# Performance work log

Hardware: AMD Instinct MI355X
Metric: run time of the kernel (lower is better)

Reference implementation:

```python
import jax, jax.numpy as jnp
import numpy as np

N_NODES = 50000
N_EDGES = 800000
F_IN = 128
HID = 128
N_GRAPHS = 256


def setup_inputs() -> dict:
    key = jax.random.key(0)
    ks = jax.random.split(key, 12)
    gx = jax.random.normal(ks[0], (N_NODES, F_IN), dtype=jnp.float32)
    edge_index = jax.random.randint(ks[1], (2, N_EDGES), 0, N_NODES, dtype=jnp.int64)
    batch = jnp.sort(jax.random.randint(ks[2], (N_NODES,), 0, N_GRAPHS, dtype=jnp.int64))
    edge_attr = jax.random.uniform(ks[3], (N_EDGES,), dtype=jnp.float32)
    s1 = 1.0 / np.sqrt(F_IN)
    s2 = 1.0 / np.sqrt(HID)
    W1 = jax.random.uniform(ks[4], (F_IN, HID), jnp.float32, -s1, s1)
    b1 = jnp.zeros((HID,), jnp.float32)
    W2 = jax.random.uniform(ks[5], (HID, HID), jnp.float32, -s2, s2)
    b2 = jnp.zeros((HID,), jnp.float32)
    W3 = jax.random.uniform(ks[6], (HID, HID), jnp.float32, -s2, s2)
    b3 = jnp.zeros((HID,), jnp.float32)
    return {"gx": gx, "edge_index": edge_index, "batch": batch, "edge_attr": edge_attr,
            "W1": W1, "b1": b1, "W2": W2, "b2": b2, "W3": W3, "b3": b3}


def _gcn_conv(x, W, b, row, col, edge_weight, n_nodes):
    # PyG GCNConv with add_self_loops=False:
    #   deg[i] = sum of edge_weight over edges with dst == i
    #   norm_e = deg^{-1/2}[row] * w_e * deg^{-1/2}[col]
    #   out[i] = sum_{e: col_e == i} norm_e * (x @ W)[row_e] + b
    deg = jax.ops.segment_sum(edge_weight, col, num_segments=n_nodes)
    dinv = jnp.where(deg > 0, jax.lax.rsqrt(deg), 0.0)
    norm = dinv[row] * edge_weight * dinv[col]  # [E]
    h = x @ W  # [N, H]
    msg = h[row] * norm[:, None]  # [E, H] gather + scale
    out = jax.ops.segment_sum(msg, col, num_segments=n_nodes)  # scatter-add
    return out + b


def reference(gx, edge_index, batch, edge_attr, W1, b1, W2, b2, W3, b3):
    row, col = edge_index[0], edge_index[1]
    n = gx.shape[0]
    # dropout layers are in eval mode (identity) for a deterministic reference
    h = jax.nn.relu(_gcn_conv(gx, W1, b1, row, col, edge_attr, n))
    h = jax.nn.relu(_gcn_conv(h, W2, b2, row, col, edge_attr, n))
    h = _gcn_conv(h, W3, b3, row, col, edge_attr, n)
    readout = jax.ops.segment_sum(h, batch, num_segments=N_GRAPHS)  # global_add_pool
    return h, readout
```

## Files before the change

### kernel.cpp

```cpp
#include <hip/hip_runtime.h>

#define FEAT 128

typedef __attribute__((ext_vector_type(8))) short short8;
typedef __attribute__((ext_vector_type(4))) float f32x4;

__device__ __forceinline__ unsigned int bf16rtn(float f) {
    unsigned int u = __float_as_uint(f);
    return (u + 0x7fffu + ((u >> 16) & 1u)) >> 16;
}
__device__ __forceinline__ float bf16tof(unsigned int h) { return __uint_as_float(h << 16); }
__device__ __forceinline__ float bf16lo(unsigned int v) { return __uint_as_float(v << 16); }
__device__ __forceinline__ float bf16hi(unsigned int v) { return __uint_as_float(v & 0xffff0000u); }

__global__ __launch_bounds__(256) void hist_kernel(const int* __restrict__ col,
                                                   int* __restrict__ ghist,
                                                   const float* __restrict__ W0,
                                                   const float* __restrict__ W1,
                                                   const float* __restrict__ W2,
                                                   unsigned short* __restrict__ Whi,
                                                   unsigned short* __restrict__ Wlo,
                                                   int E, int nblk, int nbuck) {
    __shared__ int h[256];
    const int t = threadIdx.x, b = blockIdx.x;
// ... 76 lines not shown
    if (t < nbuck) {
        int idx = t * nblk + b;
        cur[t] = gsc[idx] + sbs[idx >> 8];
    }
    __syncthreads();
    const int base = b * 4096;
#pragma unroll
    for (int i = 0; i < 16; ++i) {
        int e = base + i * 256 + t;
        if (e < E) {
            int c = col[e];
            int slot = atomicAdd(&cur[c >> 8], 1);
            bedge[slot] = make_uint2(((unsigned)c << 16) | (unsigned)row[e],
                                     __float_as_uint(ew[e]));
        }
    }
}

__global__ __launch_bounds__(256) void bucket_kernel(const uint2* __restrict__ bedge,
                                                     const int* __restrict__ gsc,
                                                     const int* __restrict__ bsum,
                                                     int* __restrict__ rowptr,
                                                     float* __restrict__ dinv,
                                                     uint2* __restrict__ sedge,
                                                     int N, int E, int nblk, int nbuck, int snb) {
    __shared__ int sbs[256];
    __shared__ int lcnt[256];
    __shared__ float lw[256];
    __shared__ int lscan[256];
    __shared__ int lcur[256];
    __shared__ float ldv[256];

    const int d = blockIdx.x, t = threadIdx.x;
    local_bsum_scan(bsum, snb, sbs, t);
    const int i0 = d * nblk;
    const int base = gsc[i0] + sbs[i0 >> 8];
    int end;
    if (d == nbuck - 1) end = E;
    else {
        const int i1 = (d + 1) * nblk;
        end = gsc[i1] + sbs[i1 >> 8];
    }

    lcnt[t] = 0;
    lw[t] = 0.f;
    __syncthreads();
    for (int i = base + t; i < end; i += 256) {
        uint2 p = bedge[i];
        int c = (p.x >> 16) & 255;
        atomicAdd(&lcnt[c], 1);
        atomicAdd(&lw[c], __uint_as_float(p.y));
    }
    __syncthreads();
    int own = lcnt[t];
    lscan[t] = own;
    for (int off = 1; off < 256; off <<= 1) {
        __syncthreads();
        int v = (t >= off) ? lscan[t - off] : 0;
        __syncthreads();
        lscan[t] += v;
    }
    __syncthreads();
    int excl = lscan[t] - own;
    lcur[t] = base + excl;
    float wsum = lw[t];
    float dv = (wsum > 0.f) ? rsqrtf(wsum) : 0.f;
    ldv[t] = dv;
    int node = d * 256 + t;
    if (node < N) {
        rowptr[node] = base + excl;
        dinv[node] = dv;
    }
    if (d == nbuck - 1 && t == 0) rowptr[N] = E;
    __syncthreads();
    for (int i = base + t; i < end; i += 256) {
        uint2 p = bedge[i];
        int c = (p.x >> 16) & 255;
        int slot = atomicAdd(&lcur[c], 1);
        sedge[slot] = make_uint2(p.x & 0xFFFFu,
                                 __float_as_uint(__uint_as_float(p.y) * ldv[c]));
    }
}

__global__ __launch_bounds__(256) void gemm_mfma_kernel(
    const float* __restrict__ X,
    const unsigned short* __restrict__ Wthi, const unsigned short* __restrict__ Wtlo,
    const float* __restrict__ dinv,
    unsigned int* __restrict__ hb,
    int N)
{
    __shared__ unsigned short wh[64 * 128];
    __shared__ unsigned short wl[64 * 128];

    const int tid = threadIdx.x;
    const int r0 = blockIdx.x * 64;
    const int cb = blockIdx.y;

#pragma unroll
    for (int it = 0; it < 4; ++it) {
        int idx = it * 256 + tid;
        int c = idx >> 4;
        int k8 = (idx & 15) * 8;
        int sw = k8 ^ ((c & 7) << 3);
        size_t src = (size_t)(cb * 64 + c) * FEAT + k8;
        *(short8*)&wh[c * 128 + sw] = *(const short8*)(Wthi + src);
        *(short8*)&wl[c * 128 + sw] = *(const short8*)(Wtlo + src);
    }
    __syncthreads();

    const int lane = tid & 63;
    const int wv = tid >> 6;
    const int m = lane & 15;
    const int quad = lane >> 4;
    const int arow = wv * 16 + m;
    const int grow = r0 + arow;
    const float* xrow = X + (size_t)grow * FEAT;

    f32x4 acc[4];
#pragma unroll
    for (int ct = 0; ct < 4; ++ct) acc[ct] = (f32x4){0.f, 0.f, 0.f, 0.f};

#pragma unroll
    for (int kt = 0; kt < 4; ++kt) {
        const int k0 = kt * 32 + quad * 8;
        float4 va = make_float4(0.f, 0.f, 0.f, 0.f);
        float4 vb = make_float4(0.f, 0.f, 0.f, 0.f);
        if (grow < N) {
            va = *(const float4*)(xrow + k0);
            vb = *(const float4*)(xrow + k0 + 4);
        }
        unsigned int h0 = bf16rtn(va.x), h1 = bf16rtn(va.y);
        unsigned int h2 = bf16rtn(va.z), h3 = bf16rtn(va.w);
        unsigned int h4 = bf16rtn(vb.x), h5 = bf16rtn(vb.y);
        unsigned int h6 = bf16rtn(vb.z), h7 = bf16rtn(vb.w);
        short8 ah, al;
        ah[0] = (short)h0; ah[1] = (short)h1; ah[2] = (short)h2; ah[3] = (short)h3;
        ah[4] = (short)h4; ah[5] = (short)h5; ah[6] = (short)h6; ah[7] = (short)h7;
        al[0] = (short)bf16rtn(va.x - bf16tof(h0));
        al[1] = (short)bf16rtn(va.y - bf16tof(h1));
        al[2] = (short)bf16rtn(va.z - bf16tof(h2));
        al[3] = (short)bf16rtn(va.w - bf16tof(h3));
        al[4] = (short)bf16rtn(vb.x - bf16tof(h4));
        al[5] = (short)bf16rtn(vb.y - bf16tof(h5));
        al[6] = (short)bf16rtn(vb.z - bf16tof(h6));
        al[7] = (short)bf16rtn(vb.w - bf16tof(h7));
#pragma unroll
        for (int ct = 0; ct < 4; ++ct) {
            int bc = ct * 16 + m;
            int bw = k0 ^ ((bc & 7) << 3);
            short8 bh = *(const short8*)&wh[bc * 128 + bw];
            short8 bl = *(const short8*)&wl[bc * 128 + bw];
            acc[ct] = __builtin_amdgcn_mfma_f32_16x16x32_bf16(ah, bh, acc[ct], 0, 0, 0);
            acc[ct] = __builtin_amdgcn_mfma_f32_16x16x32_bf16(ah, bl, acc[ct], 0, 0, 0);
            acc[ct] = __builtin_amdgcn_mfma_f32_16x16x32_bf16(al, bh, acc[ct], 0, 0, 0);
        }
    }

    const int rbase = wv * 16 + quad * 4;
    const int grb = r0 + rbase;
    float dv0, dv1, dv2, dv3;
    if (grb + 3 < N) {
        float4 d4 = *(const float4*)(dinv + grb);
        dv0 = d4.x; dv1 = d4.y; dv2 = d4.z; dv3 = d4.w;
    } else {
        dv0 = (grb + 0 < N) ? dinv[grb + 0] : 0.f;
        dv1 = (grb + 1 < N) ? dinv[grb + 1] : 0.f;
        dv2 = (grb + 2 < N) ? dinv[grb + 2] : 0.f;
        dv3 = (grb + 3 < N) ? dinv[grb + 3] : 0.f;
    }

    __syncthreads();
    unsigned short* cl = wh;
#pragma unroll
    for (int ct = 0; ct < 4; ++ct) {
        cl[(rbase + 0) * 72 + ct * 16 + m] = (unsigned short)bf16rtn(acc[ct][0] * dv0);
        cl[(rbase + 1) * 72 + ct * 16 + m] = (unsigned short)bf16rtn(acc[ct][1] * dv1);
        cl[(rbase + 2) * 72 + ct * 16 + m] = (unsigned short)bf16rtn(acc[ct][2] * dv2);
        cl[(rbase + 3) * 72 + ct * 16 + m] = (unsigned short)bf16rtn(acc[ct][3] * dv3);
    }
    __syncthreads();
#pragma unroll
    for (int it = 0; it < 2; ++it) {
        int idx = it * 256 + tid;
        int r = idx >> 3;
        int c4 = (idx & 7) * 4;
        int gr = r0 + r;
        if (gr < N) {
            uint4 pv = *(const uint4*)&cl[r * 72 + c4 * 2];
            *(uint4*)(hb + (size_t)gr * 64 + cb * 32 + c4) = pv;
        }
    }
}

template <int RELU>
__global__ __launch_bounds__(256) void agg_kernel(
    const int* __restrict__ rowptr, const uint2* __restrict__ sedge,
    const uint4* __restrict__ hb4,
    const float* __restrict__ bias,
    float* __restrict__ outX, int N)
{
    const int node = blockIdx.x * 16 + (threadIdx.x >> 4);
    if (node >= N) return;
    const int j = threadIdx.x & 15;
    const int s = rowptr[node];
    const int e = rowptr[node + 1];

    float a0 = 0.f, a1 = 0.f, a2 = 0.f, a3 = 0.f;
    float a4 = 0.f, a5 = 0.f, a6 = 0.f, a7 = 0.f;

    for (int gb = s; gb < e; gb += 8) {
        uint2 m0, m1, m2, m3, m4, m5, m6, m7;
        if (gb + 8 <= e) {
            m0 = sedge[gb + 0]; m1 = sedge[gb + 1];
            m2 = sedge[gb + 2]; m3 = sedge[gb + 3];
            m4 = sedge[gb + 4]; m5 = sedge[gb + 5];
            m6 = sedge[gb + 6]; m7 = sedge[gb + 7];
        } else {
            const uint2 z = make_uint2(0u, 0u);
            m0 = (gb + 0 < e) ? sedge[gb + 0] : z;
            m1 = (gb + 1 < e) ? sedge[gb + 1] : z;
            m2 = (gb + 2 < e) ? sedge[gb + 2] : z;
            m3 = (gb + 3 < e) ? sedge[gb + 3] : z;
            m4 = (gb + 4 < e) ? sedge[gb + 4] : z;
            m5 = (gb + 5 < e) ? sedge[gb + 5] : z;
            m6 = (gb + 6 < e) ? sedge[gb + 6] : z;
            m7 = (gb + 7 < e) ? sedge[gb + 7] : z;
        }
        uint4 v0 = hb4[(size_t)m0.x * 16 + j];
        uint4 v1 = hb4[(size_t)m1.x * 16 + j];
        uint4 v2 = hb4[(size_t)m2.x * 16 + j];
        uint4 v3 = hb4[(size_t)m3.x * 16 + j];
        uint4 v4 = hb4[(size_t)m4.x * 16 + j];
        uint4 v5 = hb4[(size_t)m5.x * 16 + j];
        uint4 v6 = hb4[(size_t)m6.x * 16 + j];
        uint4 v7 = hb4[(size_t)m7.x * 16 + j];
        float w0 = __uint_as_float(m0.y), w1 = __uint_as_float(m1.y);
        float w2 = __uint_as_float(m2.y), w3 = __uint_as_float(m3.y);
        float w4 = __uint_as_float(m4.y), w5 = __uint_as_float(m5.y);
        float w6 = __uint_as_float(m6.y), w7 = __uint_as_float(m7.y);
        a0 = fmaf(w0, bf16lo(v0.x), a0); a1 = fmaf(w0, bf16hi(v0.x), a1);
        a2 = fmaf(w0, bf16lo(v0.y), a2); a3 = fmaf(w0, bf16hi(v0.y), a3);
        a4 = fmaf(w0, bf16lo(v0.z), a4); a5 = fmaf(w0, bf16hi(v0.z), a5);
        a6 = fmaf(w0, bf16lo(v0.w), a6); a7 = fmaf(w0, bf16hi(v0.w), a7);
        a0 = fmaf(w1, bf16lo(v1.x), a0); a1 = fmaf(w1, bf16hi(v1.x), a1);
        a2 = fmaf(w1, bf16lo(v1.y), a2); a3 = fmaf(w1, bf16hi(v1.y), a3);
        a4 = fmaf(w1, bf16lo(v1.z), a4); a5 = fmaf(w1, bf16hi(v1.z), a5);
        a6 = fmaf(w1, bf16lo(v1.w), a6); a7 = fmaf(w1, bf16hi(v1.w), a7);
        a0 = fmaf(w2, bf16lo(v2.x), a0); a1 = fmaf(w2, bf16hi(v2.x), a1);
        a2 = fmaf(w2, bf16lo(v2.y), a2); a3 = fmaf(w2, bf16hi(v2.y), a3);
        a4 = fmaf(w2, bf16lo(v2.z), a4); a5 = fmaf(w2, bf16hi(v2.z), a5);
        a6 = fmaf(w2, bf16lo(v2.w), a6); a7 = fmaf(w2, bf16hi(v2.w), a7);
        a0 = fmaf(w3, bf16lo(v3.x), a0); a1 = fmaf(w3, bf16hi(v3.x), a1);
        a2 = fmaf(w3, bf16lo(v3.y), a2); a3 = fmaf(w3, bf16hi(v3.y), a3);
        a4 = fmaf(w3, bf16lo(v3.z), a4); a5 = fmaf(w3, bf16hi(v3.z), a5);
        a6 = fmaf(w3, bf16lo(v3.w), a6); a7 = fmaf(w3, bf16hi(v3.w), a7);
        a0 = fmaf(w4, bf16lo(v4.x), a0); a1 = fmaf(w4, bf16hi(v4.x), a1);
        a2 = fmaf(w4, bf16lo(v4.y), a2); a3 = fmaf(w4, bf16hi(v4.y), a3);
        a4 = fmaf(w4, bf16lo(v4.z), a4); a5 = fmaf(w4, bf16hi(v4.z), a5);
        a6 = fmaf(w4, bf16lo(v4.w), a6); a7 = fmaf(w4, bf16hi(v4.w), a7);
        a0 = fmaf(w5, bf16lo(v5.x), a0); a1 = fmaf(w5, bf16hi(v5.x), a1);
        a2 = fmaf(w5, bf16lo(v5.y), a2); a3 = fmaf(w5, bf16hi(v5.y), a3);
        a4 = fmaf(w5, bf16lo(v5.z), a4); a5 = fmaf(w5, bf16hi(v5.z), a5);
        a6 = fmaf(w5, bf16lo(v5.w), a6); a7 = fmaf(w5, bf16hi(v5.w), a7);
        a0 = fmaf(w6, bf16lo(v6.x), a0); a1 = fmaf(w6, bf16hi(v6.x), a1);
        a2 = fmaf(w6, bf16lo(v6.y), a2); a3 = fmaf(w6, bf16hi(v6.y), a3);
        a4 = fmaf(w6, bf16lo(v6.z), a4); a5 = fmaf(w6, bf16hi(v6.z), a5);
        a6 = fmaf(w6, bf16lo(v6.w), a6); a7 = fmaf(w6, bf16hi(v6.w), a7);
        a0 = fmaf(w7, bf16lo(v7.x), a0); a1 = fmaf(w7, bf16hi(v7.x), a1);
        a2 = fmaf(w7, bf16lo(v7.y), a2); a3 = fmaf(w7, bf16hi(v7.y), a3);
        a4 = fmaf(w7, bf16lo(v7.z), a4); a5 = fmaf(w7, bf16hi(v7.z), a5);
        a6 = fmaf(w7, bf16lo(v7.w), a6); a7 = fmaf(w7, bf16hi(v7.w), a7);
    }

    float4 bv0 = ((const float4*)bias)[j * 2];
    float4 bv1 = ((const float4*)bias)[j * 2 + 1];
    a0 += bv0.x; a1 += bv0.y; a2 += bv0.z; a3 += bv0.w;
    a4 += bv1.x; a5 += bv1.y; a6 += bv1.z; a7 += bv1.w;
    if (RELU) {
        a0 = fmaxf(a0, 0.f); a1 = fmaxf(a1, 0.f);
        a2 = fmaxf(a2, 0.f); a3 = fmaxf(a3, 0.f);
        a4 = fmaxf(a4, 0.f); a5 = fmaxf(a5, 0.f);
        a6 = fmaxf(a6, 0.f); a7 = fmaxf(a7, 0.f);
    }
    *(float4*)(outX + (size_t)node * FEAT + j * 8)     = make_float4(a0, a1, a2, a3);
    *(float4*)(outX + (size_t)node * FEAT + j * 8 + 4) = make_float4(a4, a5, a6, a7);
}

__global__ __launch_bounds__(256) void readout_kernel(const float* __restrict__ h,
                                                      const int* __restrict__ batch,
                                                      float* __restrict__ ro, int N) {
    __shared__ float part[128];
    const int g = blockIdx.x;
    const int j = threadIdx.x & 127;
    const int half = threadIdx.x >> 7;
    int lo = 0, hi = N;
    while (lo < hi) { int mid = (lo + hi) >> 1; if (batch[mid] < g) lo = mid + 1; else hi = mid; }
    int lo2 = lo, hi2 = N;
    while (lo2 < hi2) { int mid = (lo2 + hi2) >> 1; if (batch[mid] < g + 1) lo2 = mid + 1; else hi2 = mid; }

    float s0 = 0.f, s1 = 0.f;
    int n = lo + half;
    for (; n + 2 < lo2; n += 4) {
        s0 += h[(size_t)n * FEAT + j];
        s1 += h[(size_t)(n + 2) * FEAT + j];
    }
    if (n < lo2) s0 += h[(size_t)n * FEAT + j];
    float s = s0 + s1;
    if (half == 1) part[j] = s;
    __syncthreads();
    if (half == 0) ro[(size_t)g * FEAT + j] = s + part[j];
}

static inline size_t align256(size_t x) { return (x + 255) & ~(size_t)255; }

extern "C" void kernel_launch(void* const* d_in, const int* in_sizes, int n_in,
                              void* d_out, int out_size, void* d_ws, size_t ws_size,
                              hipStream_t stream) {
    const float* gx    = (const float*)d_in[0];
    const int*   ei    = (const int*)d_in[1];
    const int*   batch = (const int*)d_in[2];
    const float* ew    = (const float*)d_in[3];
    const float* W1 = (const float*)d_in[4];
    const float* b1 = (const float*)d_in[5];
    const float* W2 = (const float*)d_in[6];
    const float* b2 = (const float*)d_in[7];
    const float* W3 = (const float*)d_in[8];
    const float* b3 = (const float*)d_in[9];

    const int N = in_sizes[0] / FEAT;
    const int E = in_sizes[3];
    const int G = (out_size - N * FEAT) / FEAT;

    const int* row = ei;
    const int* col = ei + E;

    const int nbuck = (N + 255) >> 8;
    const int nblk  = (E + 4095) >> 12;
    const int M     = nbuck * nblk;
    const int snb   = (M + 255) / 256;

    char* ws = (char*)d_ws;
    int*   rowptr = (int*)ws;         ws += align256((size_t)(N + 1) * 4);
    float* dinv   = (float*)ws;       ws += align256((size_t)N * 4);
    int*   ghist  = (int*)ws;         ws += align256((size_t)M * 4);
    int*   gsc    = (int*)ws;         ws += align256((size_t)M * 4);
    int*   bsum   = (int*)ws;         ws += align256(256 * 4);
    uint2* bedge  = (uint2*)ws;       ws += align256((size_t)E * 8);
    uint2* sedge  = (uint2*)ws;       ws += align256((size_t)E * 8);
    unsigned int* hb = (unsigned int*)ws;  ws += align256((size_t)N * 64 * 4);
    float* bufX   = (float*)ws;       ws += align256((size_t)N * FEAT * 4);
    unsigned short* Wh = (unsigned short*)ws; ws += align256((size_t)3 * 16384 * 2);
    unsigned short* Wl = (unsigned short*)ws; ws += align256((size_t)3 * 16384 * 2);

    float* h_out = (float*)d_out;
    float* ro    = h_out + (size_t)N * FEAT;

    hist_kernel<<<nblk + 16, 256, 0, stream>>>(col, ghist, W1, W2, W3, Wh, Wl, E, nblk, nbuck);
    scan_block_kernel<<<snb, 256, 0, stream>>>(ghist, gsc, bsum, M);
    scatter1_kernel<<<nblk, 256, 0, stream>>>(row, col, ew, gsc, bsum, bedge, E, nblk, nbuck, snb);
    bucket_kernel<<<nbuck, 256, 0, stream>>>(bedge, gsc, bsum, rowptr, dinv, sedge, N, E, nblk, nbuck, snb);

    dim3 ggrid((N + 63) / 64, 2);
    const int ablocks = (N + 15) / 16;
    const uint4* hb4 = (const uint4*)hb;

    gemm_mfma_kernel<<<ggrid, 256, 0, stream>>>(gx, Wh, Wl, dinv, hb, N);
    agg_kernel<1><<<ablocks, 256, 0, stream>>>(rowptr, sedge, hb4, b1, bufX, N);
    gemm_mfma_kernel<<<ggrid, 256, 0, stream>>>(bufX, Wh + 16384, Wl + 16384, dinv, hb, N);
    agg_kernel<1><<<ablocks, 256, 0, stream>>>(rowptr, sedge, hb4, b2, bufX, N);
    gemm_mfma_kernel<<<ggrid, 256, 0, stream>>>(bufX, Wh + 32768, Wl + 32768, dinv, hb, N);
    agg_kernel<0><<<ablocks, 256, 0, stream>>>(rowptr, sedge, hb4, b3, h_out, N);
    readout_kernel<<<G, 256, 0, stream>>>(h_out, batch, ro, N);
}
```

Baseline: 285.7 us.

## Emit bf16 hi/lo split from aggregation and compute both column halves per GEMM block

After: 294.9 us. 1.03x slower.

```diff
diff --git a/kernel.cpp b/kernel.cpp
--- a/kernel.cpp
+++ b/kernel.cpp
@@ -182,8 +182,10 @@
     }
 }
 
+template <int FRAG_IN>
 __global__ __launch_bounds__(256) void gemm_mfma_kernel(
     const float* __restrict__ X,
+    const unsigned short* __restrict__ Xh, const unsigned short* __restrict__ Xl,
     const unsigned short* __restrict__ Wthi, const unsigned short* __restrict__ Wtlo,
     const float* __restrict__ dinv,
     unsigned int* __restrict__ hb,
@@ -194,65 +196,47 @@
 
     const int tid = threadIdx.x;
     const int r0 = blockIdx.x * 64;
-    const int cb = blockIdx.y;
-
-#pragma unroll
-    for (int it = 0; it < 4; ++it) {
-        int idx = it * 256 + tid;
-        int c = idx >> 4;
-        int k8 = (idx & 15) * 8;
-        int sw = k8 ^ ((c & 7) << 3);
-        size_t src = (size_t)(cb * 64 + c) * FEAT + k8;
-        *(short8*)&wh[c * 128 + sw] = *(const short8*)(Wthi + src);
-        *(short8*)&wl[c * 128 + sw] = *(const short8*)(Wtlo + src);
-    }
-    __syncthreads();
-
     const int lane = tid & 63;
     const int wv = tid >> 6;
     const int m = lane & 15;
     const int quad = lane >> 4;
     const int arow = wv * 16 + m;
     const int grow = r0 + arow;
-    const float* xrow = X + (size_t)grow * FEAT;
-
-    f32x4 acc[4];
-#pragma unroll
-    for (int ct = 0; ct < 4; ++ct) acc[ct] = (f32x4){0.f, 0.f, 0.f, 0.f};
-
+
+    short8 AH[4], AL[4];
 #pragma unroll
     for (int kt = 0; kt < 4; ++kt) {
         const int k0 = kt * 32 + quad * 8;
-        float4 va = make_float4(0.f, 0.f, 0.f, 0.f);
-        float4 vb = make_float4(0.f, 0.f, 0.f, 0.f);
-        if (grow < N) {
-            va = *(const float4*)(xrow + k0);
-            vb = *(const float4*)(xrow + k0 + 4);
-        }
-        unsigned int h0 = bf16rtn(va.x), h1 = bf16rtn(va.y);
-        unsigned int h2 = bf16rtn(va.z), h3 = bf16rtn(va.w);
-        unsigned int h4 = bf16rtn(vb.x), h5 = bf16rtn(vb.y);
-        unsigned int h6 = bf16rtn(vb.z), h7 = bf16rtn(vb.w);
-        short8 ah, al;
-        ah[0] = (short)h0; ah[1] = (short)h1; ah[2] = (short)h2; ah[3] = (short)h3;
-        ah[4] = (short)h4; ah[5] = (short)h5; ah[6] = (short)h6; ah[7] = (short)h7;
-        al[0] = (short)bf16rtn(va.x - bf16tof(h0));
-        al[1] = (short)bf16rtn(va.y - bf16tof(h1));
-        al[2] = (short)bf16rtn(va.z - bf16tof(h2));
-        al[3] = (short)bf16rtn(va.w - bf16tof(h3));
-        al[4] = (short)bf16rtn(vb.x - bf16tof(h4));
-        al[5] = (short)bf16rtn(vb.y - bf16tof(h5));
-        al[6] = (short)bf16rtn(vb.z - bf16tof(h6));
-        al[7] = (short)bf16rtn(vb.w - bf16tof(h7));
-#pragma unroll
-        for (int ct = 0; ct < 4; ++ct) {
-            int bc = ct * 16 + m;
-            int bw = k0 ^ ((bc & 7) << 3);
-            short8 bh = *(const short8*)&wh[bc * 128 + bw];
-            short8 bl = *(const short8*)&wl[bc * 128 + bw];
-            acc[ct] = __builtin_amdgcn_mfma_f32_16x16x32_bf16(ah, bh, acc[ct], 0, 0, 0);
-            acc[ct] = __builtin_amdgcn_mfma_f32_16x16x32_bf16(ah, bl, acc[ct], 0, 0, 0);
-            acc[ct] = __builtin_amdgcn_mfma_f32_16x16x32_bf16(al, bh, acc[ct], 0, 0, 0);
+        if (FRAG_IN) {
+            short8 z = {0, 0, 0, 0, 0, 0, 0, 0};
+            AH[kt] = z; AL[kt] = z;
+            if (grow < N) {
+                AH[kt] = *(const short8*)(Xh + (size_t)grow * FEAT + k0);
+                AL[kt] = *(const short8*)(Xl + (size_t)grow * FEAT + k0);
+            }
+        } else {
+            float4 va = make_float4(0.f, 0.f, 0.f, 0.f);
+            float4 vb = make_float4(0.f, 0.f, 0.f, 0.f);
+            if (grow < N) {
+                va = *(const float4*)(X + (size_t)grow * FEAT + k0);
+                vb = *(const float4*)(X + (size_t)grow * FEAT + k0 + 4);
+            }
+            unsigned int h0 = bf16rtn(va.x), h1 = bf16rtn(va.y);
+            unsigned int h2 = bf16rtn(va.z), h3 = bf16rtn(va.w);
+            unsigned int h4 = bf16rtn(vb.x), h5 = bf16rtn(vb.y);
+            unsigned int h6 = bf16rtn(vb.z), h7 = bf16rtn(vb.w);
+            short8 ah, al;
+            ah[0] = (short)h0; ah[1] = (short)h1; ah[2] = (short)h2; ah[3] = (short)h3;
+            ah[4] = (short)h4; ah[5] = (short)h5; ah[6] = (short)h6; ah[7] = (short)h7;
+            al[0] = (short)bf16rtn(va.x - bf16tof(h0));
+            al[1] = (short)bf16rtn(va.y - bf16tof(h1));
+            al[2] = (short)bf16rtn(va.z - bf16tof(h2));
+            al[3] = (short)bf16rtn(va.w - bf16tof(h3));
+            al[4] = (short)bf16rtn(vb.x - bf16tof(h4));
+            al[5] = (short)bf16rtn(vb.y - bf16tof(h5));
+            al[6] = (short)bf16rtn(vb.z - bf16tof(h6));
+            al[7] = (short)bf16rtn(vb.w - bf16tof(h7));
+            AH[kt] = ah; AL[kt] = al;
         }
     }
 
@@ -269,35 +253,71 @@
         dv3 = (grb + 3 < N) ? dinv[grb + 3] : 0.f;
     }
 
-    __syncthreads();
-    unsigned short* cl = wh;
-#pragma unroll
-    for (int ct = 0; ct < 4; ++ct) {
-        cl[(rbase + 0) * 72 + ct * 16 + m] = (unsigned short)bf16rtn(acc[ct][0] * dv0);
-        cl[(rbase + 1) * 72 + ct * 16 + m] = (unsigned short)bf16rtn(acc[ct][1] * dv1);
-        cl[(rbase + 2) * 72 + ct * 16 + m] = (unsigned short)bf16rtn(acc[ct][2] * dv2);
-        cl[(rbase + 3) * 72 + ct * 16 + m] = (unsigned short)bf16rtn(acc[ct][3] * dv3);
-    }
-    __syncthreads();
-#pragma unroll
-    for (int it = 0; it < 2; ++it) {
-        int idx = it * 256 + tid;
-        int r = idx >> 3;
-        int c4 = (idx & 7) * 4;
-        int gr = r0 + r;
-        if (gr < N) {
-            uint4 pv = *(const uint4*)&cl[r * 72 + c4 * 2];
-            *(uint4*)(hb + (size_t)gr * 64 + cb * 32 + c4) = pv;
-        }
-    }
-}
-
-template <int RELU>
+#pragma unroll
+    for (int cb = 0; cb < 2; ++cb) {
+        __syncthreads();
+#pragma unroll
+        for (int it = 0; it < 4; ++it) {
+            int idx = it * 256 + tid;
+            int c = idx >> 4;
+            int k8 = (idx & 15) * 8;
+            int sw = k8 ^ ((c & 7) << 3);
+            size_t src = (size_t)(cb * 64 + c) * FEAT + k8;
+            *(short8*)&wh[c * 128 + sw] = *(const short8*)(Wthi + src);
+            *(short8*)&wl[c * 128 + sw] = *(const short8*)(Wtlo + src);
+        }
+        __syncthreads();
+
+        f32x4 acc[4];
+#pragma unroll
+        for (int ct = 0; ct < 4; ++ct) acc[ct] = (f32x4){0.f, 0.f, 0.f, 0.f};
+
+#pragma unroll
+        for (int kt = 0; kt < 4; ++kt) {
+            const int k0 = kt * 32 + quad * 8;
+#pragma unroll
+            for (int ct = 0; ct < 4; ++ct) {
+                int bc = ct * 16 + m;
+                int bw = k0 ^ ((bc & 7) << 3);
+                short8 bh = *(const short8*)&wh[bc * 128 + bw];
+                short8 bl = *(const short8*)&wl[bc * 128 + bw];
+                acc[ct] = __builtin_amdgcn_mfma_f32_16x16x32_bf16(AH[kt], bh, acc[ct], 0, 0, 0);
+                acc[ct] = __builtin_amdgcn_mfma_f32_16x16x32_bf16(AH[kt], bl, acc[ct], 0, 0, 0);
+                acc[ct] = __builtin_amdgcn_mfma_f32_16x16x32_bf16(AL[kt], bh, acc[ct], 0, 0, 0);
+            }
+        }
+
+        __syncthreads();
+        unsigned short* cl = wl;
+#pragma unroll
+        for (int ct = 0; ct < 4; ++ct) {
+            cl[(rbase + 0) * 72 + ct * 16 + m] = (unsigned short)bf16rtn(acc[ct][0] * dv0);
+            cl[(rbase + 1) * 72 + ct * 16 + m] = (unsigned short)bf16rtn(acc[ct][1] * dv1);
+            cl[(rbase + 2) * 72 + ct * 16 + m] = (unsigned short)bf16rtn(acc[ct][2] * dv2);
+            cl[(rbase + 3) * 72 + ct * 16 + m] = (unsigned short)bf16rtn(acc[ct][3] * dv3);
+        }
+        __syncthreads();
+#pragma unroll
+        for (int it = 0; it < 2; ++it) {
+            int idx = it * 256 + tid;
+            int r = idx >> 3;
+            int c4 = (idx & 7) * 4;
+            int gr = r0 + r;
+            if (gr < N) {
+                uint4 pv = *(const uint4*)&cl[r * 72 + c4 * 2];
+                *(uint4*)(hb + (size_t)gr * 64 + cb * 32 + c4) = pv;
+            }
+        }
+    }
+}
+
+template <int MODE>
 __global__ __launch_bounds__(256) void agg_kernel(
     const int* __restrict__ rowptr, const uint2* __restrict__ sedge,
     const uint4* __restrict__ hb4,
     const float* __restrict__ bias,
-    float* __restrict__ outX, int N)
+    float* __restrict__ outX,
+    unsigned short* __restrict__ Xh, unsigned short* __restrict__ Xl, int N)
 {
     const int node = blockIdx.x * 16 + (threadIdx.x >> 4);
     if (node >= N) return;
@@ -376,14 +396,28 @@
     float4 bv1 = ((const float4*)bias)[j * 2 + 1];
     a0 += bv0.x; a1 += bv0.y; a2 += bv0.z; a3 += bv0.w;
     a4 += bv1.x; a5 += bv1.y; a6 += bv1.z; a7 += bv1.w;
-    if (RELU) {
+
+    if (MODE == 0) {
         a0 = fmaxf(a0, 0.f); a1 = fmaxf(a1, 0.f);
         a2 = fmaxf(a2, 0.f); a3 = fmaxf(a3, 0.f);
         a4 = fmaxf(a4, 0.f); a5 = fmaxf(a5, 0.f);
         a6 = fmaxf(a6, 0.f); a7 = fmaxf(a7, 0.f);
-    }
-    *(float4*)(outX + (size_t)node * FEAT + j * 8)     = make_float4(a0, a1, a2, a3);
-    *(float4*)(outX + (size_t)node * FEAT + j * 8 + 4) = make_float4(a4, a5, a6, a7);
+        unsigned int h0 = bf16rtn(a0), h1 = bf16rtn(a1), h2 = bf16rtn(a2), h3 = bf16rtn(a3);
+        unsigned int h4 = bf16rtn(a4), h5 = bf16rtn(a5), h6 = bf16rtn(a6), h7 = bf16rtn(a7);
+        uint4 hv = make_uint4(h0 | (h1 << 16), h2 | (h3 << 16),
+                              h4 | (h5 << 16), h6 | (h7 << 16));
+        unsigned int l0 = bf16rtn(a0 - bf16tof(h0)), l1 = bf16rtn(a1 - bf16tof(h1));
+        unsigned int l2 = bf16rtn(a2 - bf16tof(h2)), l3 = bf16rtn(a3 - bf16tof(h3));
+        unsigned int l4 = bf16rtn(a4 - bf16tof(h4)), l5 = bf16rtn(a5 - bf16tof(h5));
+        unsigned int l6 = bf16rtn(a6 - bf16tof(h6)), l7 = bf16rtn(a7 - bf16tof(h7));
+        uint4 lv = make_uint4(l0 | (l1 << 16), l2 | (l3 << 16),
+                              l4 | (l5 << 16), l6 | (l7 << 16));
+        *(uint4*)(Xh + (size_t)node * FEAT + j * 8) = hv;
+        *(uint4*)(Xl + (size_t)node * FEAT + j * 8) = lv;
+    } else {
+        *(float4*)(outX + (size_t)node * FEAT + j * 8)     = make_float4(a0, a1, a2, a3);
+        *(float4*)(outX + (size_t)node * FEAT + j * 8 + 4) = make_float4(a4, a5, a6, a7);
+    }
 }
 
 __global__ __launch_bounds__(256) void readout_kernel(const float* __restrict__ h,
@@ -448,7 +482,8 @@
     uint2* bedge  = (uint2*)ws;       ws += align256((size_t)E * 8);
     uint2* sedge  = (uint2*)ws;       ws += align256((size_t)E * 8);
     unsigned int* hb = (unsigned int*)ws;  ws += align256((size_t)N * 64 * 4);
-    float* bufX   = (float*)ws;       ws += align256((size_t)N * FEAT * 4);
+    unsigned short* Xh = (unsigned short*)ws; ws += align256((size_t)N * FEAT * 2);
+    unsigned short* Xl = (unsigned short*)ws; ws += align256((size_t)N * FEAT * 2);
     unsigned short* Wh = (unsigned short*)ws; ws += align256((size_t)3 * 16384 * 2);
     unsigned short* Wl = (unsigned short*)ws; ws += align256((size_t)3 * 16384 * 2);
 
@@ -460,15 +495,15 @@
     scatter1_kernel<<<nblk, 256, 0, stream>>>(row, col, ew, gsc, bsum, bedge, E, nblk, nbuck, snb);
     bucket_kernel<<<nbuck, 256, 0, stream>>>(bedge, gsc, bsum, rowptr, dinv, sedge, N, E, nblk, nbuck, snb);
 
-    dim3 ggrid((N + 63) / 64, 2);
+    const int gblocks = (N + 63) / 64;
     const int ablocks = (N + 15) / 16;
     const uint4* hb4 = (const uint4*)hb;
 
-    gemm_mfma_kernel<<<ggrid, 256, 0, stream>>>(gx, Wh, Wl, dinv, hb, N);
-    agg_kernel<1><<<ablocks, 256, 0, stream>>>(rowptr, sedge, hb4, b1, bufX, N);
-    gemm_mfma_kernel<<<ggrid, 256, 0, stream>>>(bufX, Wh + 16384, Wl + 16384, dinv, hb, N);
-    agg_kernel<1><<<ablocks, 256, 0, stream>>>(rowptr, sedge, hb4, b2, bufX, N);
-    gemm_mfma_kernel<<<ggrid, 256, 0, stream>>>(bufX, Wh + 32768, Wl + 32768, dinv, hb, N);
-    agg_kernel<0><<<ablocks, 256, 0, stream>>>(rowptr, sedge, hb4, b3, h_out, N);
+    gemm_mfma_kernel<0><<<gblocks, 256, 0, stream>>>(gx, nullptr, nullptr, Wh, Wl, dinv, hb, N);
+    agg_kernel<0><<<ablocks, 256, 0, stream>>>(rowptr, sedge, hb4, b1, nullptr, Xh, Xl, N);
+    gemm_mfma_kernel<1><<<gblocks, 256, 0, stream>>>(nullptr, Xh, Xl, Wh + 16384, Wl + 16384, dinv, hb, N);
+    agg_kernel<0><<<ablocks, 256, 0, stream>>>(rowptr, sedge, hb4, b2, nullptr, Xh, Xl, N);
+    gemm_mfma_kernel<1><<<gblocks, 256, 0, stream>>>(nullptr, Xh, Xl, Wh + 32768, Wl + 32768, dinv, hb, N);
+    agg_kernel<1><<<ablocks, 256, 0, stream>>>(rowptr, sedge, hb4, b3, h_out, nullptr, nullptr, N);
     readout_kernel<<<G, 256, 0, stream>>>(h_out, batch, ro, N);
 }
```

## Fuse aggregation with next layer's MFMA GEMM, ping-pong bf16 buffers

Applied to the files above, without the earlier changes.

Result: slower. 298.2 us (+4.4%).

```diff
diff --git a/kernel.cpp b/kernel.cpp
--- a/kernel.cpp
+++ b/kernel.cpp
@@ -288,6 +288,189 @@
         if (gr < N) {
             uint4 pv = *(const uint4*)&cl[r * 72 + c4 * 2];
             *(uint4*)(hb + (size_t)gr * 64 + cb * 32 + c4) = pv;
+        }
+    }
+}
+
+__global__ __launch_bounds__(256) void agg_gemm_kernel(
+    const int* __restrict__ rowptr, const uint2* __restrict__ sedge,
+    const uint4* __restrict__ hb_in,
+    const float* __restrict__ bias,
+    const unsigned short* __restrict__ Wthi, const unsigned short* __restrict__ Wtlo,
+    const float* __restrict__ dinv,
+    unsigned int* __restrict__ hb_out,
+    int N)
+{
+    __shared__ unsigned short xh[16 * 128];
+    __shared__ unsigned short xl[16 * 128];
+    __shared__ unsigned short cl[16 * 136];
+
+    const int tid = threadIdx.x;
+    const int r0 = blockIdx.x * 16;
+    const int nloc = tid >> 4;
+    const int node = r0 + nloc;
+    const int j = tid & 15;
+    const bool active = node < N;
+    int s = 0, e = 0;
+    if (active) { s = rowptr[node]; e = rowptr[node + 1]; }
+
+    float a0 = 0.f, a1 = 0.f, a2 = 0.f, a3 = 0.f;
+    float a4 = 0.f, a5 = 0.f, a6 = 0.f, a7 = 0.f;
+
+    for (int gb = s; gb < e; gb += 8) {
+        uint2 m0, m1, m2, m3, m4, m5, m6, m7;
+        if (gb + 8 <= e) {
+            m0 = sedge[gb + 0]; m1 = sedge[gb + 1];
+            m2 = sedge[gb + 2]; m3 = sedge[gb + 3];
+            m4 = sedge[gb + 4]; m5 = sedge[gb + 5];
+            m6 = sedge[gb + 6]; m7 = sedge[gb + 7];
+        } else {
+            const uint2 z = make_uint2(0u, 0u);
+            m0 = (gb + 0 < e) ? sedge[gb + 0] : z;
+            m1 = (gb + 1 < e) ? sedge[gb + 1] : z;
+            m2 = (gb + 2 < e) ? sedge[gb + 2] : z;
+            m3 = (gb + 3 < e) ? sedge[gb + 3] : z;
+            m4 = (gb + 4 < e) ? sedge[gb + 4] : z;
+            m5 = (gb + 5 < e) ? sedge[gb + 5] : z;
+            m6 = (gb + 6 < e) ? sedge[gb + 6] : z;
+            m7 = (gb + 7 < e) ? sedge[gb + 7] : z;
+        }
+        uint4 v0 = hb_in[(size_t)m0.x * 16 + j];
+        uint4 v1 = hb_in[(size_t)m1.x * 16 + j];
+        uint4 v2 = hb_in[(size_t)m2.x * 16 + j];
+        uint4 v3 = hb_in[(size_t)m3.x * 16 + j];
+        uint4 v4 = hb_in[(size_t)m4.x * 16 + j];
+        uint4 v5 = hb_in[(size_t)m5.x * 16 + j];
+        uint4 v6 = hb_in[(size_t)m6.x * 16 + j];
+        uint4 v7 = hb_in[(size_t)m7.x * 16 + j];
+        float w0 = __uint_as_float(m0.y), w1 = __uint_as_float(m1.y);
+        float w2 = __uint_as_float(m2.y), w3 = __uint_as_float(m3.y);
+        float w4 = __uint_as_float(m4.y), w5 = __uint_as_float(m5.y);
+        float w6 = __uint_as_float(m6.y), w7 = __uint_as_float(m7.y);
+        a0 = fmaf(w0, bf16lo(v0.x), a0); a1 = fmaf(w0, bf16hi(v0.x), a1);
+        a2 = fmaf(w0, bf16lo(v0.y), a2); a3 = fmaf(w0, bf16hi(v0.y), a3);
+        a4 = fmaf(w0, bf16lo(v0.z), a4); a5 = fmaf(w0, bf16hi(v0.z), a5);
+        a6 = fmaf(w0, bf16lo(v0.w), a6); a7 = fmaf(w0, bf16hi(v0.w), a7);
+        a0 = fmaf(w1, bf16lo(v1.x), a0); a1 = fmaf(w1, bf16hi(v1.x), a1);
+        a2 = fmaf(w1, bf16lo(v1.y), a2); a3 = fmaf(w1, bf16hi(v1.y), a3);
+        a4 = fmaf(w1, bf16lo(v1.z), a4); a5 = fmaf(w1, bf16hi(v1.z), a5);
+        a6 = fmaf(w1, bf16lo(v1.w), a6); a7 = fmaf(w1, bf16hi(v1.w), a7);
+        a0 = fmaf(w2, bf16lo(v2.x), a0); a1 = fmaf(w2, bf16hi(v2.x), a1);
+        a2 = fmaf(w2, bf16lo(v2.y), a2); a3 = fmaf(w2, bf16hi(v2.y), a3);
+        a4 = fmaf(w2, bf16lo(v2.z), a4); a5 = fmaf(w2, bf16hi(v2.z), a5);
+        a6 = fmaf(w2, bf16lo(v2.w), a6); a7 = fmaf(w2, bf16hi(v2.w), a7);
+        a0 = fmaf(w3, bf16lo(v3.x), a0); a1 = fmaf(w3, bf16hi(v3.x), a1);
+        a2 = fmaf(w3, bf16lo(v3.y), a2); a3 = fmaf(w3, bf16hi(v3.y), a3);
+        a4 = fmaf(w3, bf16lo(v3.z), a4); a5 = fmaf(w3, bf16hi(v3.z), a5);
+        a6 = fmaf(w3, bf16lo(v3.w), a6); a7 = fmaf(w3, bf16hi(v3.w), a7);
+        a0 = fmaf(w4, bf16lo(v4.x), a0); a1 = fmaf(w4, bf16hi(v4.x), a1);
+        a2 = fmaf(w4, bf16lo(v4.y), a2); a3 = fmaf(w4, bf16hi(v4.y), a3);
+        a4 = fmaf(w4, bf16lo(v4.z), a4); a5 = fmaf(w4, bf16hi(v4.z), a5);
+        a6 = fmaf(w4, bf16lo(v4.w), a6); a7 = fmaf(w4, bf16hi(v4.w), a7);
+        a0 = fmaf(w5, bf16lo(v5.x), a0); a1 = fmaf(w5, bf16hi(v5.x), a1);
+        a2 = fmaf(w5, bf16lo(v5.y), a2); a3 = fmaf(w5, bf16hi(v5.y), a3);
+        a4 = fmaf(w5, bf16lo(v5.z), a4); a5 = fmaf(w5, bf16hi(v5.z), a5);
+        a6 = fmaf(w5, bf16lo(v5.w), a6); a7 = fmaf(w5, bf16hi(v5.w), a7);
+        a0 = fmaf(w6, bf16lo(v6.x), a0); a1 = fmaf(w6, bf16hi(v6.x), a1);
+        a2 = fmaf(w6, bf16lo(v6.y), a2); a3 = fmaf(w6, bf16hi(v6.y), a3);
+        a4 = fmaf(w6, bf16lo(v6.z), a4); a5 = fmaf(w6, bf16hi(v6.z), a5);
+        a6 = fmaf(w6, bf16lo(v6.w), a6); a7 = fmaf(w6, bf16hi(v6.w), a7);
+        a0 = fmaf(w7, bf16lo(v7.x), a0); a1 = fmaf(w7, bf16hi(v7.x), a1);
+        a2 = fmaf(w7, bf16lo(v7.y), a2); a3 = fmaf(w7, bf16hi(v7.y), a3);
+        a4 = fmaf(w7, bf16lo(v7.z), a4); a5 = fmaf(w7, bf16hi(v7.z), a5);
+        a6 = fmaf(w7, bf16lo(v7.w), a6); a7 = fmaf(w7, bf16hi(v7.w), a7);
+    }
+
+    float4 bv0 = ((const float4*)bias)[j * 2];
+    float4 bv1 = ((const float4*)bias)[j * 2 + 1];
+    a0 = fmaxf(a0 + bv0.x, 0.f); a1 = fmaxf(a1 + bv0.y, 0.f);
+    a2 = fmaxf(a2 + bv0.z, 0.f); a3 = fmaxf(a3 + bv0.w, 0.f);
+    a4 = fmaxf(a4 + bv1.x, 0.f); a5 = fmaxf(a5 + bv1.y, 0.f);
+    a6 = fmaxf(a6 + bv1.z, 0.f); a7 = fmaxf(a7 + bv1.w, 0.f);
+
+    unsigned int h0 = bf16rtn(a0), h1 = bf16rtn(a1), h2 = bf16rtn(a2), h3 = bf16rtn(a3);
+    unsigned int h4 = bf16rtn(a4), h5 = bf16rtn(a5), h6 = bf16rtn(a6), h7 = bf16rtn(a7);
+    short8 hv, lv;
+    hv[0] = (short)h0; hv[1] = (short)h1; hv[2] = (short)h2; hv[3] = (short)h3;
+    hv[4] = (short)h4; hv[5] = (short)h5; hv[6] = (short)h6; hv[7] = (short)h7;
+    lv[0] = (short)bf16rtn(a0 - bf16tof(h0));
+    lv[1] = (short)bf16rtn(a1 - bf16tof(h1));
+    lv[2] = (short)bf16rtn(a2 - bf16tof(h2));
+    lv[3] = (short)bf16rtn(a3 - bf16tof(h3));
+    lv[4] = (short)bf16rtn(a4 - bf16tof(h4));
+    lv[5] = (short)bf16rtn(a5 - bf16tof(h5));
+    lv[6] = (short)bf16rtn(a6 - bf16tof(h6));
+    lv[7] = (short)bf16rtn(a7 - bf16tof(h7));
+    {
+        int sw = (j * 8) ^ ((nloc & 7) << 3);
+        *(short8*)&xh[nloc * 128 + sw] = hv;
+        *(short8*)&xl[nloc * 128 + sw] = lv;
+    }
+    __syncthreads();
+
+    const int lane = tid & 63;
+    const int w = tid >> 6;
+    const int m = lane & 15;
+    const int quad = lane >> 4;
+
+    short8 AH[4], AL[4];
+#pragma unroll
+    for (int kt = 0; kt < 4; ++kt) {
+        int aw = (kt * 32 + quad * 8) ^ ((m & 7) << 3);
+        AH[kt] = *(const short8*)&xh[m * 128 + aw];
+        AL[kt] = *(const short8*)&xl[m * 128 + aw];
+    }
+
+    f32x4 acc0 = (f32x4){0.f, 0.f, 0.f, 0.f};
+    f32x4 acc1 = (f32x4){0.f, 0.f, 0.f, 0.f};
+#pragma unroll
+    for (int kt = 0; kt < 4; ++kt) {
+        const int k0 = kt * 32 + quad * 8;
+        const size_t bc0 = (size_t)(w * 32 + m) * FEAT + k0;
+        const size_t bc1 = (size_t)(w * 32 + 16 + m) * FEAT + k0;
+        short8 bh0 = *(const short8*)(Wthi + bc0);
+        short8 bl0 = *(const short8*)(Wtlo + bc0);
+        short8 bh1 = *(const short8*)(Wthi + bc1);
+        short8 bl1 = *(const short8*)(Wtlo + bc1);
+        acc0 = __builtin_amdgcn_mfma_f32_16x16x32_bf16(AH[kt], bh0, acc0, 0, 0, 0);
+        acc1 = __builtin_amdgcn_mfma_f32_16x16x32_bf16(AH[kt], bh1, acc1, 0, 0, 0);
+        acc0 = __builtin_amdgcn_mfma_f32_16x16x32_bf16(AH[kt], bl0, acc0, 0, 0, 0);
+        acc1 = __builtin_amdgcn_mfma_f32_16x16x32_bf16(AH[kt], bl1, acc1, 0, 0, 0);
+        acc0 = __builtin_amdgcn_mfma_f32_16x16x32_bf16(AL[kt], bh0, acc0, 0, 0, 0);
+        acc1 = __builtin_amdgcn_mfma_f32_16x16x32_bf16(AL[kt], bh1, acc1, 0, 0, 0);
+    }
+
+    const int grb = r0 + quad * 4;
+    float dv0, dv1, dv2, dv3;
+    if (grb + 3 < N) {
+        float4 d4 = *(const float4*)(dinv + grb);
+        dv0 = d4.x; dv1 = d4.y; dv2 = d4.z; dv3 = d4.w;
+    } else {
+        dv0 = (grb + 0 < N) ? dinv[grb + 0] : 0.f;
+        dv1 = (grb + 1 < N) ? dinv[grb + 1] : 0.f;
+        dv2 = (grb + 2 < N) ? dinv[grb + 2] : 0.f;
+        dv3 = (grb + 3 < N) ? dinv[grb + 3] : 0.f;
+    }
+    {
+        const int cb0 = w * 32 + m;
+        const int cb1 = w * 32 + 16 + m;
+        cl[(quad * 4 + 0) * 136 + cb0] = (unsigned short)bf16rtn(acc0[0] * dv0);
+        cl[(quad * 4 + 1) * 136 + cb0] = (unsigned short)bf16rtn(acc0[1] * dv1);
+        cl[(quad * 4 + 2) * 136 + cb0] = (unsigned short)bf16rtn(acc0[2] * dv2);
+        cl[(quad * 4 + 3) * 136 + cb0] = (unsigned short)bf16rtn(acc0[3] * dv3);
+        cl[(quad * 4 + 0) * 136 + cb1] = (unsigned short)bf16rtn(acc1[0] * dv0);
+        cl[(quad * 4 + 1) * 136 + cb1] = (unsigned short)bf16rtn(acc1[1] * dv1);
+        cl[(quad * 4 + 2) * 136 + cb1] = (unsigned short)bf16rtn(acc1[2] * dv2);
+        cl[(quad * 4 + 3) * 136 + cb1] = (unsigned short)bf16rtn(acc1[3] * dv3);
+    }
+    __syncthreads();
+    {
+        int r = tid >> 4;
+        int c8 = (tid & 15) * 8;
+        int gr = r0 + r;
+        if (gr < N) {
+            uint4 pv = *(const uint4*)&cl[r * 136 + c8];
+            *(uint4*)(hb_out + (size_t)gr * 64 + (tid & 15) * 4) = pv;
         }
     }
 }
@@ -447,8 +630,8 @@
     int*   bsum   = (int*)ws;         ws += align256(256 * 4);
     uint2* bedge  = (uint2*)ws;       ws += align256((size_t)E * 8);
     uint2* sedge  = (uint2*)ws;       ws += align256((size_t)E * 8);
-    unsigned int* hb = (unsigned int*)ws;  ws += align256((size_t)N * 64 * 4);
-    float* bufX   = (float*)ws;       ws += align256((size_t)N * FEAT * 4);
+    unsigned int* hbA = (unsigned int*)ws;  ws += align256((size_t)N * 64 * 4);
+    unsigned int* hbB = (unsigned int*)ws;  ws += align256((size_t)N * 64 * 4);
     unsigned short* Wh = (unsigned short*)ws; ws += align256((size_t)3 * 16384 * 2);
     unsigned short* Wl = (unsigned short*)ws; ws += align256((size_t)3 * 16384 * 2);
 
@@ -460,15 +643,13 @@
     scatter1_kernel<<<nblk, 256, 0, stream>>>(row, col, ew, gsc, bsum, bedge, E, nblk, nbuck, snb);
     bucket_kernel<<<nbuck, 256, 0, stream>>>(bedge, gsc, bsum, rowptr, dinv, sedge, N, E, nblk, nbuck, snb);
 
-    dim3 ggrid((N + 63) / 64, 2);
     const int ablocks = (N + 15) / 16;
-    const uint4* hb4 = (const uint4*)hb;
-
-    gemm_mfma_kernel<<<ggrid, 256, 0, stream>>>(gx, Wh, Wl, dinv, hb, N);
-    agg_kernel<1><<<ablocks, 256, 0, stream>>>(rowptr, sedge, hb4, b1, bufX, N);
-    gemm_mfma_kernel<<<ggrid, 256, 0, stream>>>(bufX, Wh + 16384, Wl + 16384, dinv, hb, N);
-    agg_kernel<1><<<ablocks, 256, 0, stream>>>(rowptr, sedge, hb4, b2, bufX, N);
-    gemm_mfma_kernel<<<ggrid, 256, 0, stream>>>(bufX, Wh + 32768, Wl + 32768, dinv, hb, N);
-    agg_kernel<0><<<ablocks, 256, 0, stream>>>(rowptr, sedge, hb4, b3, h_out, N);
+
+    gemm_mfma_kernel<<<dim3((N + 63) / 64, 2), 256, 0, stream>>>(gx, Wh, Wl, dinv, hbA, N);
+    agg_gemm_kernel<<<ablocks, 256, 0, stream>>>(rowptr, sedge, (const uint4*)hbA, b1,
+                                                 Wh + 16384, Wl + 16384, dinv, hbB, N);
+    agg_gemm_kernel<<<ablocks, 256, 0, stream>>>(rowptr, sedge, (const uint4*)hbB, b2,
+                                                 Wh + 32768, Wl + 32768, dinv, hbA, N);
+    agg_kernel<0><<<ablocks, 256, 0, stream>>>(rowptr, sedge, (const uint4*)hbA, b3, h_out, N);
     readout_kernel<<<G, 256, 0, stream>>>(h_out, batch, ro, N);
 }
```

## Split bf16 features into column quarters and parallelize edges within node groups

Applied to the files above, without the earlier changes.

Result: slower. 431.2 us (+50.9%).

```diff
diff --git a/kernel.cpp b/kernel.cpp
--- a/kernel.cpp
+++ b/kernel.cpp
@@ -186,7 +186,7 @@
     const float* __restrict__ X,
     const unsigned short* __restrict__ Wthi, const unsigned short* __restrict__ Wtlo,
     const float* __restrict__ dinv,
-    unsigned int* __restrict__ hb,
+    unsigned int* __restrict__ hbq,
     int N)
 {
     __shared__ unsigned short wh[64 * 128];
@@ -287,57 +287,52 @@
         int gr = r0 + r;
         if (gr < N) {
             uint4 pv = *(const uint4*)&cl[r * 72 + c4 * 2];
-            *(uint4*)(hb + (size_t)gr * 64 + cb * 32 + c4) = pv;
-        }
-    }
-}
-
-template <int RELU>
+            int col_u = cb * 32 + c4;
+            int q = col_u >> 4;
+            int wq = col_u & 15;
+            *(uint4*)(hbq + ((size_t)q * N + gr) * 16 + wq) = pv;
+        }
+    }
+}
+
+template <int MODE>
 __global__ __launch_bounds__(256) void agg_kernel(
     const int* __restrict__ rowptr, const uint2* __restrict__ sedge,
-    const uint4* __restrict__ hb4,
+    const unsigned int* __restrict__ hbq,
     const float* __restrict__ bias,
-    float* __restrict__ outX, int N)
+    float* __restrict__ outX, int N, int nb16)
 {
-    const int node = blockIdx.x * 16 + (threadIdx.x >> 4);
+    const int q  = blockIdx.x / nb16;
+    const int nb = blockIdx.x - q * nb16;
+    const int node = nb * 16 + (threadIdx.x >> 4);
     if (node >= N) return;
-    const int j = threadIdx.x & 15;
+    const int j  = threadIdx.x & 15;
+    const int fl = j & 3;
+    const int es = j >> 2;
     const int s = rowptr[node];
     const int e = rowptr[node + 1];
+    const unsigned int* hq = hbq + (size_t)q * N * 16;
 
     float a0 = 0.f, a1 = 0.f, a2 = 0.f, a3 = 0.f;
     float a4 = 0.f, a5 = 0.f, a6 = 0.f, a7 = 0.f;
 
-    for (int gb = s; gb < e; gb += 8) {
-        uint2 m0, m1, m2, m3, m4, m5, m6, m7;
-        if (gb + 8 <= e) {
-            m0 = sedge[gb + 0]; m1 = sedge[gb + 1];
-            m2 = sedge[gb + 2]; m3 = sedge[gb + 3];
-            m4 = sedge[gb + 4]; m5 = sedge[gb + 5];
-            m6 = sedge[gb + 6]; m7 = sedge[gb + 7];
-        } else {
-            const uint2 z = make_uint2(0u, 0u);
-            m0 = (gb + 0 < e) ? sedge[gb + 0] : z;
-            m1 = (gb + 1 < e) ? sedge[gb + 1] : z;
-            m2 = (gb + 2 < e) ? sedge[gb + 2] : z;
-            m3 = (gb + 3 < e) ? sedge[gb + 3] : z;
-            m4 = (gb + 4 < e) ? sedge[gb + 4] : z;
-            m5 = (gb + 5 < e) ? sedge[gb + 5] : z;
-            m6 = (gb + 6 < e) ? sedge[gb + 6] : z;
-            m7 = (gb + 7 < e) ? sedge[gb + 7] : z;
-        }
-        uint4 v0 = hb4[(size_t)m0.x * 16 + j];
-        uint4 v1 = hb4[(size_t)m1.x * 16 + j];
-        uint4 v2 = hb4[(size_t)m2.x * 16 + j];
-        uint4 v3 = hb4[(size_t)m3.x * 16 + j];
-        uint4 v4 = hb4[(size_t)m4.x * 16 + j];
-        uint4 v5 = hb4[(size_t)m5.x * 16 + j];
-        uint4 v6 = hb4[(size_t)m6.x * 16 + j];
-        uint4 v7 = hb4[(size_t)m7.x * 16 + j];
+    for (int gb = s; gb < e; gb += 16) {
+        const int e0 = gb + es * 4 + 0;
+        const int e1 = gb + es * 4 + 1;
+        const int e2 = gb + es * 4 + 2;
+        const int e3 = gb + es * 4 + 3;
+        const uint2 z = make_uint2(0u, 0u);
+        const uint4 z4 = make_uint4(0u, 0u, 0u, 0u);
+        uint2 m0 = (e0 < e) ? sedge[e0] : z;
+        uint2 m1 = (e1 < e) ? sedge[e1] : z;
+        uint2 m2 = (e2 < e) ? sedge[e2] : z;
+        uint2 m3 = (e3 < e) ? sedge[e3] : z;
+        uint4 v0 = (e0 < e) ? *(const uint4*)(hq + (size_t)m0.x * 16 + fl * 4) : z4;
+        uint4 v1 = (e1 < e) ? *(const uint4*)(hq + (size_t)m1.x * 16 + fl * 4) : z4;
+        uint4 v2 = (e2 < e) ? *(const uint4*)(hq + (size_t)m2.x * 16 + fl * 4) : z4;
+        uint4 v3 = (e3 < e) ? *(const uint4*)(hq + (size_t)m3.x * 16 + fl * 4) : z4;
         float w0 = __uint_as_float(m0.y), w1 = __uint_as_float(m1.y);
         float w2 = __uint_as_float(m2.y), w3 = __uint_as_float(m3.y);
-        float w4 = __uint_as_float(m4.y), w5 = __uint_as_float(m5.y);
-        float w6 = __uint_as_float(m6.y), w7 = __uint_as_float(m7.y);
         a0 = fmaf(w0, bf16lo(v0.x), a0); a1 = fmaf(w0, bf16hi(v0.x), a1);
         a2 = fmaf(w0, bf16lo(v0.y), a2); a3 = fmaf(w0, bf16hi(v0.y), a3);
         a4 = fmaf(w0, bf16lo(v0.z), a4); a5 = fmaf(w0, bf16hi(v0.z), a5);
@@ -354,36 +349,32 @@
         a2 = fmaf(w3, bf16lo(v3.y), a2); a3 = fmaf(w3, bf16hi(v3.y), a3);
         a4 = fmaf(w3, bf16lo(v3.z), a4); a5 = fmaf(w3, bf16hi(v3.z), a5);
         a6 = fmaf(w3, bf16lo(v3.w), a6); a7 = fmaf(w3, bf16hi(v3.w), a7);
-        a0 = fmaf(w4, bf16lo(v4.x), a0); a1 = fmaf(w4, bf16hi(v4.x), a1);
-        a2 = fmaf(w4, bf16lo(v4.y), a2); a3 = fmaf(w4, bf16hi(v4.y), a3);
-        a4 = fmaf(w4, bf16lo(v4.z), a4); a5 = fmaf(w4, bf16hi(v4.z), a5);
-        a6 = fmaf(w4, bf16lo(v4.w), a6); a7 = fmaf(w4, bf16hi(v4.w), a7);
-        a0 = fmaf(w5, bf16lo(v5.x), a0); a1 = fmaf(w5, bf16hi(v5.x), a1);
-        a2 = fmaf(w5, bf16lo(v5.y), a2); a3 = fmaf(w5, bf16hi(v5.y), a3);
-        a4 = fmaf(w5, bf16lo(v5.z), a4); a5 = fmaf(w5, bf16hi(v5.z), a5);
-        a6 = fmaf(w5, bf16lo(v5.w), a6); a7 = fmaf(w5, bf16hi(v5.w), a7);
-        a0 = fmaf(w6, bf16lo(v6.x), a0); a1 = fmaf(w6, bf16hi(v6.x), a1);
-        a2 = fmaf(w6, bf16lo(v6.y), a2); a3 = fmaf(w6, bf16hi(v6.y), a3);
-        a4 = fmaf(w6, bf16lo(v6.z), a4); a5 = fmaf(w6, bf16hi(v6.z), a5);
-        a6 = fmaf(w6, bf16lo(v6.w), a6); a7 = fmaf(w6, bf16hi(v6.w), a7);
-        a0 = fmaf(w7, bf16lo(v7.x), a0); a1 = fmaf(w7, bf16hi(v7.x), a1);
-        a2 = fmaf(w7, bf16lo(v7.y), a2); a3 = fmaf(w7, bf16hi(v7.y), a3);
-        a4 = fmaf(w7, bf16lo(v7.z), a4); a5 = fmaf(w7, bf16hi(v7.z), a5);
-        a6 = fmaf(w7, bf16lo(v7.w), a6); a7 = fmaf(w7, bf16hi(v7.w), a7);
-    }
-
-    float4 bv0 = ((const float4*)bias)[j * 2];
-    float4 bv1 = ((const float4*)bias)[j * 2 + 1];
-    a0 += bv0.x; a1 += bv0.y; a2 += bv0.z; a3 += bv0.w;
-    a4 += bv1.x; a5 += bv1.y; a6 += bv1.z; a7 += bv1.w;
-    if (RELU) {
-        a0 = fmaxf(a0, 0.f); a1 = fmaxf(a1, 0.f);
-        a2 = fmaxf(a2, 0.f); a3 = fmaxf(a3, 0.f);
-        a4 = fmaxf(a4, 0.f); a5 = fmaxf(a5, 0.f);
-        a6 = fmaxf(a6, 0.f); a7 = fmaxf(a7, 0.f);
-    }
-    *(float4*)(outX + (size_t)node * FEAT + j * 8)     = make_float4(a0, a1, a2, a3);
-    *(float4*)(outX + (size_t)node * FEAT + j * 8 + 4) = make_float4(a4, a5, a6, a7);
+    }
+
+    a0 += __shfl_xor(a0, 4); a0 += __shfl_xor(a0, 8);
+    a1 += __shfl_xor(a1, 4); a1 += __shfl_xor(a1, 8);
+    a2 += __shfl_xor(a2, 4); a2 += __shfl_xor(a2, 8);
+    a3 += __shfl_xor(a3, 4); a3 += __shfl_xor(a3, 8);
+    a4 += __shfl_xor(a4, 4); a4 += __shfl_xor(a4, 8);
+    a5 += __shfl_xor(a5, 4); a5 += __shfl_xor(a5, 8);
+    a6 += __shfl_xor(a6, 4); a6 += __shfl_xor(a6, 8);
+    a7 += __shfl_xor(a7, 4); a7 += __shfl_xor(a7, 8);
+
+    if (es == 0) {
+        float4 bv0 = ((const float4*)bias)[q * 8 + fl * 2];
+        float4 bv1 = ((const float4*)bias)[q * 8 + fl * 2 + 1];
+        a0 += bv0.x; a1 += bv0.y; a2 += bv0.z; a3 += bv0.w;
+        a4 += bv1.x; a5 += bv1.y; a6 += bv1.z; a7 += bv1.w;
+        if (MODE == 0) {
+            a0 = fmaxf(a0, 0.f); a1 = fmaxf(a1, 0.f);
+            a2 = fmaxf(a2, 0.f); a3 = fmaxf(a3, 0.f);
+            a4 = fmaxf(a4, 0.f); a5 = fmaxf(a5, 0.f);
+            a6 = fmaxf(a6, 0.f); a7 = fmaxf(a7, 0.f);
+        }
+        float* dst = outX + (size_t)node * FEAT + q * 32 + fl * 8;
+        *(float4*)(dst)     = make_float4(a0, a1, a2, a3);
+        *(float4*)(dst + 4) = make_float4(a4, a5, a6, a7);
+    }
 }
 
 __global__ __launch_bounds__(256) void readout_kernel(const float* __restrict__ h,
@@ -447,7 +438,7 @@
     int*   bsum   = (int*)ws;         ws += align256(256 * 4);
     uint2* bedge  = (uint2*)ws;       ws += align256((size_t)E * 8);
     uint2* sedge  = (uint2*)ws;       ws += align256((size_t)E * 8);
-    unsigned int* hb = (unsigned int*)ws;  ws += align256((size_t)N * 64 * 4);
+    unsigned int* hbq = (unsigned int*)ws;  ws += align256((size_t)N * 64 * 4);
     float* bufX   = (float*)ws;       ws += align256((size_t)N * FEAT * 4);
     unsigned short* Wh = (unsigned short*)ws; ws += align256((size_t)3 * 16384 * 2);
     unsigned short* Wl = (unsigned short*)ws; ws += align256((size_t)3 * 16384 * 2);
@@ -461,14 +452,14 @@
     bucket_kernel<<<nbuck, 256, 0, stream>>>(bedge, gsc, bsum, rowptr, dinv, sedge, N, E, nblk, nbuck, snb);
 
     dim3 ggrid((N + 63) / 64, 2);
-    const int ablocks = (N + 15) / 16;
-    const uint4* hb4 = (const uint4*)hb;
-
-    gemm_mfma_kernel<<<ggrid, 256, 0, stream>>>(gx, Wh, Wl, dinv, hb, N);
-    agg_kernel<1><<<ablocks, 256, 0, stream>>>(rowptr, sedge, hb4, b1, bufX, N);
-    gemm_mfma_kernel<<<ggrid, 256, 0, stream>>>(bufX, Wh + 16384, Wl + 16384, dinv, hb, N);
-    agg_kernel<1><<<ablocks, 256, 0, stream>>>(rowptr, sedge, hb4, b2, bufX, N);
-    gemm_mfma_kernel<<<ggrid, 256, 0, stream>>>(bufX, Wh + 32768, Wl + 32768, dinv, hb, N);
-    agg_kernel<0><<<ablocks, 256, 0, stream>>>(rowptr, sedge, hb4, b3, h_out, N);
+    const int nb16 = (N + 15) / 16;
+    const int ablocks = 4 * nb16;
+
+    gemm_mfma_kernel<<<ggrid, 256, 0, stream>>>(gx, Wh, Wl, dinv, hbq, N);
+    agg_kernel<0><<<ablocks, 256, 0, stream>>>(rowptr, sedge, hbq, b1, bufX, N, nb16);
+    gemm_mfma_kernel<<<ggrid, 256, 0, stream>>>(bufX, Wh + 16384, Wl + 16384, dinv, hbq, N);
+    agg_kernel<0><<<ablocks, 256, 0, stream>>>(rowptr, sedge, hbq, b2, bufX, N, nb16);
+    gemm_mfma_kernel<<<ggrid, 256, 0, stream>>>(bufX, Wh + 32768, Wl + 32768, dinv, hbq, N);
+    agg_kernel<1><<<ablocks, 256, 0, stream>>>(rowptr, sedge, hbq, b3, h_out, N, nb16);
     readout_kernel<<<G, 256, 0, stream>>>(h_out, batch, ro, N);
 }
```
